# Kernel optimization log

Hardware: AMD Instinct MI355X
Metric: run time of the kernel (lower is better)

## Reference

```python
import jax, jax.numpy as jnp
import numpy as np

BOS = 1          # BOS_TOK_IDX
PAD = 0          # PAD_TOK_IDX (embedding padding row zeroed)
NL = 2           # n_layers (both decoder and encoder)
H_DEC = 1024     # decoder hidden = enc.emb_size
H_ENC = 512      # encoder hidden per direction (out_size = 1024)


def lstm_cell(x, h, c, Wih, Whh, bih, bhh):
    # PyTorch gate order: i, f, g, o
    gates = x @ Wih.T + h @ Whh.T + bih + bhh
    i, f, g, o = jnp.split(gates, 4, axis=-1)
    c = jax.nn.sigmoid(f) * c + jax.nn.sigmoid(i) * jnp.tanh(g)
    h = jax.nn.sigmoid(o) * jnp.tanh(c)
    return h, c


def setup_inputs() -> dict:
    key = jax.random.key(0)
    ks = jax.random.split(key, 20)
    B, T_ENC, V, E = 32, 128, 32000, 512
    sd = 1.0 / np.sqrt(H_DEC)
    se = 1.0 / np.sqrt(H_ENC)
    u = lambda k, shape, s: jax.random.uniform(k, shape, jnp.float32, -s, s)
    emb_W = jax.random.normal(ks[0], (V, E), jnp.float32)
    emb_W = emb_W.at[PAD].set(0.0)  # padding_idx
    return {
        "enc_outs": jax.random.normal(ks[1], (B, T_ENC, 2 * H_ENC), jnp.float32),
        "enc_h": 0.1 * jax.random.normal(ks[2], (NL, B, H_DEC), jnp.float32),
        "enc_c": 0.1 * jax.random.normal(ks[3], (NL, B, H_DEC), jnp.float32),
        "max_len": 256,
        "emb_W": emb_W,
        # decoder LSTM (unidirectional, 2 layers; layer0 in=E, layer1 in=H_DEC)
        "dec_Wih0": u(ks[4], (4 * H_DEC, E), sd),
        "dec_Whh0": u(ks[5], (4 * H_DEC, H_DEC), sd),
        "dec_bih0": u(ks[6], (4 * H_DEC,), sd),
        "dec_bhh0": u(ks[7], (4 * H_DEC,), sd),
        "dec_Wih1": u(ks[8], (4 * H_DEC, H_DEC), sd),
        "dec_Whh1": u(ks[9], (4 * H_DEC, H_DEC), sd),
        "dec_bih1": u(ks[10], (4 * H_DEC,), sd),
        "dec_bhh1": u(ks[11], (4 * H_DEC,), sd),
        # encoder biLSTM, stacked [layer, dir]; input dim 1024 for both layers
        "enc_Wih": u(ks[12], (NL, 2, 4 * H_ENC, 2 * H_ENC), se),
        "enc_Whh": u(ks[13], (NL, 2, 4 * H_ENC, H_ENC), se),
        "enc_bih": u(ks[14], (NL, 2, 4 * H_ENC), se),
        "enc_bhh": u(ks[15], (NL, 2, 4 * H_ENC), se),
    }


def _run_dir(x, Wih, Whh, bih, bhh, reverse):
    # x: [B, T, D] -> ys: [B, T, H], final (h, c)
    B = x.shape[0]
    H = Whh.shape[-1]
    z = jnp.zeros((B, H), dtype=x.dtype)

    def step(carry, xt):
        h, c = lstm_cell(xt, carry[0], carry[1], Wih, Whh, bih, bhh)
        return (h, c), h

    (hT, cT), ys = jax.lax.scan(step, (z, z), jnp.swapaxes(x, 0, 1), reverse=reverse)
    return jnp.swapaxes(ys, 0, 1), hT, cT


def reference(enc_outs, enc_h, enc_c, max_len, emb_W,
              dec_Wih0, dec_Whh0, dec_bih0, dec_bhh0,
              dec_Wih1, dec_Whh1, dec_bih1, dec_bhh1,
              enc_Wih, enc_Whh, enc_bih, enc_bhh):
    B = enc_outs.shape[0]
    # dec_inps is never updated in the loop: always the BOS embedding (eval dropout = id)
    x0 = jnp.broadcast_to(emb_W[BOS], (B, emb_W.shape[1]))

    def dec_step(carry, _):
        h0, c0, h1, c1 = carry
        h0, c0 = lstm_cell(x0, h0, c0, dec_Wih0, dec_Whh0, dec_bih0, dec_bhh0)
        h1, c1 = lstm_cell(h0, h1, c1, dec_Wih1, dec_Whh1, dec_bih1, dec_bhh1)
        return (h0, c0, h1, c1), h1

    init = (enc_h[0], enc_c[0], enc_h[1], enc_c[1])
    _, result = jax.lax.scan(dec_step, init, None, length=max_len)  # [T, B, H_DEC]
    out = jnp.swapaxes(result, 0, 1)  # [B, T, H_DEC]

    # bidirectional encoder over the decoded sequence (pre_embedded, full lengths)
    for l in range(NL):
        yf, hf, cf = _run_dir(out, enc_Wih[l, 0], enc_Whh[l, 0], enc_bih[l, 0], enc_bhh[l, 0], False)
        yb, hb, cb = _run_dir(out, enc_Wih[l, 1], enc_Whh[l, 1], enc_bih[l, 1], enc_bhh[l, 1], True)
        out = jnp.concatenate([yf, yb], axis=-1)

    # to_dec_state: concat last-layer fwd/bwd states, expand over n_layers
    lnhn = jnp.concatenate([hf, hb], axis=1)  # [B, out_size]
    lncn = jnp.concatenate([cf, cb], axis=1)
    dec_h = jnp.broadcast_to(lnhn, (NL,) + lnhn.shape)
    dec_c = jnp.broadcast_to(lncn, (NL,) + lncn.shape)
    return out, dec_h, dec_c
```

## Files before the change

kernel.cpp:

```cpp
#include <hip/hip_runtime.h>


typedef _Float16 f16;
typedef _Float16 hvec8 __attribute__((ext_vector_type(8)));
typedef float fvec4 __attribute__((ext_vector_type(4)));

#define WS_H0   4096
#define WS_H1   135168
#define WS_HE   266240
#define WS_DEC  397312
#define WS_Y0   17174528

__device__ __forceinline__ fvec4 mf(hvec8 a, hvec8 b, fvec4 c) {
    return __builtin_amdgcn_mfma_f32_16x16x32_f16(a, b, c, 0, 0, 0);
}

__device__ __forceinline__ hvec8 ldb8(const float* p) {
    hvec8 h;
#pragma unroll
    for (int j = 0; j < 8; ++j) h[j] = (f16)p[j];
    return h;
}

__device__ __forceinline__ hvec8 lda8(const f16* p) {
    hvec8 v;
    asm volatile("global_load_dwordx4 %0, %1, off sc1" : "=v"(v) : "v"(p));
    return v;
}
__device__ __forceinline__ void vm_wait() {
    asm volatile("s_waitcnt vmcnt(0)" ::: "memory");
    __builtin_amdgcn_sched_barrier(0);
}

__device__ __forceinline__ void st2(f16* p, float a, float b) {
    union { f16 h[2]; unsigned u; } x;
    x.h[0] = (f16)a; x.h[1] = (f16)b;
    __hip_atomic_store((unsigned*)p, x.u, __ATOMIC_RELAXED, __HIP_MEMORY_SCOPE_AGENT);
}

__device__ __forceinline__ float sigf(float x) { return 1.f / (1.f + __expf(-x)); }
__device__ __forceinline__ float thf(float x) {
    x = fminf(15.f, fmaxf(-15.f, x));
    float e = __expf(2.f * x);
    return (e - 1.f) / (e + 1.f);
}

#define RED(t, m, w, n)  red[(((t)*16 + (m))*132) + ((w)*16) + (n)]

__device__ __forceinline__ float sum8(const float* p) {
    return ((p[0] + p[16]) + (p[32] + p[48])) + ((p[64] + p[80]) + (p[96] + p[112]));
}

__global__ void __launch_bounds__(512, 1)
seq2seq_kernel(const float* __restrict__ enc_h, const float* __restrict__ enc_c,
               const float* __restrict__ emb_W,
               const float* __restrict__ dWih0, const float* __restrict__ dWhh0,
               const float* __restrict__ dbih0, const float* __restrict__ dbhh0,
               const float* __restrict__ dWih1, const float* __restrict__ dWhh1,
               const float* __restrict__ dbih1, const float* __restrict__ dbhh1,
               const float* __restrict__ eWih, const float* __restrict__ eWhh,
               const float* __restrict__ ebih, const float* __restrict__ ebhh,
               float* __restrict__ out, char* __restrict__ ws)
{
    const int tid  = threadIdx.x;
    const int wave = tid >> 6, lane = tid & 63;
    const int wg   = blockIdx.x;
    const int bg   = wg >> 7;
    const int g    = wg & 127;
    const int n16  = lane & 15;
    const int kq   = (lane >> 4) * 8;

    unsigned* flags  = (unsigned*)(out + 8388608);
    unsigned* myflag = flags + (size_t)wg * 64;

    f16* H0  = (f16*)(ws + WS_H0);
    f16* H1  = (f16*)(ws + WS_H1);
    f16* HE  = (f16*)(ws + WS_HE);
    f16* DEC = (f16*)(ws + WS_DEC);
    f16* Y0  = (f16*)(ws + WS_Y0);

    __shared__ float red[64 * 132];
    __shared__ float cdec[2][8][16];
    __shared__ float cenc[16][16];
    __shared__ float pre0_l[32];
    __shared__ float bias1_l[32];
    __shared__ float biasE_l[64];

    unsigned cnt = 0;
    auto barpoll = [&](int base, int width, unsigned tgt) {
        if (lane == 0)
            __hip_atomic_store(myflag, tgt, __ATOMIC_RELAXED, __HIP_MEMORY_SCOPE_AGENT);
        const unsigned* p0 = flags + (size_t)(base + (lane & (width - 1))) * 64;
        for (;;) {
            unsigned a = __hip_atomic_load(p0, __ATOMIC_RELAXED, __HIP_MEMORY_SCOPE_AGENT);
            if (width > 64) {
                unsigned b = __hip_atomic_load(p0 + 64 * 64, __ATOMIC_RELAXED, __HIP_MEMORY_SCOPE_AGENT);
                a = a < b ? a : b;
                if (width > 128) {
                    unsigned c2 = __hip_atomic_load(p0 + 128 * 64, __ATOMIC_RELAXED, __HIP_MEMORY_SCOPE_AGENT);
                    unsigned d2 = __hip_atomic_load(p0 + 192 * 64, __ATOMIC_RELAXED, __HIP_MEMORY_SCOPE_AGENT);
                    a = a < c2 ? a : c2;
                    a = a < d2 ? a : d2;
                }
            }
            if (__all((int)(a >= tgt))) break;
            __builtin_amdgcn_s_sleep(1);
        }
    };

    const int u0 = g * 8;
    hvec8 bL0[2][4], bL1[2][8];
    {
        const int gate = n16 >> 2, uu = n16 & 3;
#pragma unroll
        for (int t = 0; t < 2; ++t) {
            const int r = gate * 1024 + u0 + t * 4 + uu;
#pragma unroll
            for (int s = 0; s < 4; ++s)
                bL0[t][s] = ldb8(dWhh0 + (size_t)r * 1024 + wave * 128 + s * 32 + kq);
#pragma unroll
            for (int s = 0; s < 8; ++s) {
                const int k1 = wave * 256 + s * 32;
                bL1[t][s] = (k1 < 1024)
                    ? ldb8(dWih1 + (size_t)r * 1024 + k1 + kq)
                    : ldb8(dWhh1 + (size_t)r * 1024 + (k1 - 1024) + kq);
            }
        }
    }
    if (tid < 128) {
        const int which = tid >> 6, q = tid & 63, j = q >> 4, m = q & 15;
        const int b = bg * 16 + m, u = u0 + 2 * j;
        const float* src_c = enc_c + (size_t)(which * 32 + b) * 1024 + u;
        const float* src_h = enc_h + (size_t)(which * 32 + b) * 1024 + u;
        cdec[which][2 * j][m]     = src_c[0];
        cdec[which][2 * j + 1][m] = src_c[1];
        f16* dst = which ? H1 : H0;
        st2(dst + (size_t)(32 + b) * 1024 + u, src_h[0], src_h[1]);
    }
    if (tid < 32) {
        const int t = tid >> 4, nn = tid & 15;
        const int r = (nn >> 2) * 1024 + u0 + t * 4 + (nn & 3);
        const float* x0 = emb_W + 512;
        float s = dbih0[r] + dbhh0[r];
        const float* wr = dWih0 + (size_t)r * 512;
        for (int k = 0; k < 512; ++k) s += wr[k] * x0[k];
        pre0_l[tid]  = s;
        bias1_l[tid] = dbih1[r] + dbhh1[r];
    }
    __syncthreads();
    if (wave == 0) barpoll(bg * 128, 128, ++cnt);
    __syncthreads();

    for (int tau = 0; tau <= 256; ++tau) {
        const int prd = (tau + 1) & 1;
        const int pwr = tau & 1;
        fvec4 acc[4];
#pragma unroll
        for (int i = 0; i < 4; ++i) acc[i] = 0;
        const int m = n16;
        hvec8 a0f[4], a1f[8];
        if (tau < 256) {
            const f16* a0 = H0 + (size_t)(prd * 32 + bg * 16 + m) * 1024 + wave * 128 + kq;
#pragma unroll
            for (int s = 0; s < 4; ++s) a0f[s] = lda8(a0 + s * 32);
        }
        if (tau >= 1) {
            const f16* a1 = (wave < 4)
                ? H0 + (size_t)(prd * 32 + bg * 16 + m) * 1024 + wave * 256 + kq
                : H1 + (size_t)(pwr * 32 + bg * 16 + m) * 1024 + (wave - 4) * 256 + kq;
#pragma unroll
            for (int s = 0; s < 8; ++s) a1f[s] = lda8(a1 + s * 32);
        }
        vm_wait();
        if (tau < 256) {
#pragma unroll
            for (int s = 0; s < 4; ++s) {
                acc[0] = mf(a0f[s], bL0[0][s], acc[0]);
                acc[1] = mf(a0f[s], bL0[1][s], acc[1]);
            }
        }
        if (tau >= 1) {
#pragma unroll
            for (int s = 0; s < 8; ++s) {
                acc[2] = mf(a1f[s], bL1[0][s], acc[2]);
                acc[3] = mf(a1f[s], bL1[1][s], acc[3]);
            }
        }
        {
            const int mg = lane >> 4;
#pragma unroll
            for (int t = 0; t < 4; ++t)
#pragma unroll
                for (int r = 0; r < 4; ++r)
                    RED(t, mg * 4 + r, wave, n16) = acc[t][r];
        }
        __syncthreads();
        float s0 = 0.f, s1 = 0.f;
        int   sm2 = 0, sj = 0;
        if (wave == 1 && tau < 256) {
            const int q = tid - 64;
            const int j = q >> 4, m2 = q & 15, t = j >> 1;
            float hh[2];
#pragma unroll
            for (int e = 0; e < 2; ++e) {
                const int uu = 2 * j + e, ul = uu & 3;
                const float* p = &RED(t, m2, 0, ul);
                const float gi = sum8(p)      + pre0_l[t * 16 + ul];
                const float gf = sum8(p + 4)  + pre0_l[t * 16 + 4 + ul];
                const float gg = sum8(p + 8)  + pre0_l[t * 16 + 8 + ul];
                const float go = sum8(p + 12) + pre0_l[t * 16 + 12 + ul];
                float c = cdec[0][uu][m2];
                c = sigf(gf) * c + sigf(gi) * thf(gg);
                hh[e] = sigf(go) * thf(c);
                cdec[0][uu][m2] = c;
            }
            st2(H0 + (size_t)(pwr * 32 + bg * 16 + m2) * 1024 + u0 + 2 * j, hh[0], hh[1]);
        }
        if (wave == 2 && tau >= 1) {
            const int q = tid - 128;
            const int j = q >> 4, m2 = q & 15, t = j >> 1;
            float hh[2];
#pragma unroll
            for (int e = 0; e < 2; ++e) {
                const int uu = 2 * j + e, ul = uu & 3;
                const float* p = &RED(2 + t, m2, 0, ul);
                const float gi = sum8(p)      + bias1_l[t * 16 + ul];
                const float gf = sum8(p + 4)  + bias1_l[t * 16 + 4 + ul];
                const float gg = sum8(p + 8)  + bias1_l[t * 16 + 8 + ul];
                const float go = sum8(p + 12) + bias1_l[t * 16 + 12 + ul];
                float c = cdec[1][uu][m2];
                c = sigf(gf) * c + sigf(gi) * thf(gg);
                hh[e] = sigf(go) * thf(c);
                cdec[1][uu][m2] = c;
            }
            const int b = bg * 16 + m2, u = u0 + 2 * j;
            st2(H1 + (size_t)(prd * 32 + b) * 1024 + u, hh[0], hh[1]);
            s0 = hh[0]; s1 = hh[1]; sm2 = m2; sj = j;
        }
        __syncthreads();
        if (wave == 0) {
            barpoll(bg * 128, 128, ++cnt);
        } else if (wave == 2 && tau >= 1) {
            st2(DEC + ((size_t)(tau - 1) * 32 + bg * 16 + sm2) * 1024 + u0 + 2 * sj, s0, s1);
        }
        __syncthreads();
    }

    __syncthreads();
    if (wave == 0) barpoll(0, 256, ++cnt);
    __syncthreads();
    if (wg >= 128) return;

    const int bg2 = wg >> 6;
    const int dir = (wg >> 5) & 1;
    const int ge  = wg & 31;
    const int ue0 = ge * 16;
    const int dbase = bg2 * 64 + dir * 32;
    float fdh0 = 0.f, fdh1 = 0.f, fdc0 = 0.f, fdc1 = 0.f;
    int   fdm2 = 0, fdj = 0;
    for (int l = 0; l < 2; ++l) {
        hvec8 bE[4][6];
        {
            const int gate = n16 >> 2, uu = n16 & 3;
            const float* Wih = eWih + (size_t)(l * 2 + dir) * 2048 * 1024;
            const float* Whh = eWhh + (size_t)(l * 2 + dir) * 2048 * 512;
#pragma unroll
            for (int t = 0; t < 4; ++t) {
                const int r = gate * 512 + ue0 + t * 4 + uu;
#pragma unroll
                for (int s = 0; s < 6; ++s) {
                    const int kb = wave * 192 + s * 32;
                    bE[t][s] = (kb < 1024)
                        ? ldb8(Wih + (size_t)r * 1024 + kb + kq)
                        : ldb8(Whh + (size_t)r * 512 + (kb - 1024) + kq);
                }
            }
        }
        if (tid < 64) {
            const int t = tid >> 4, nn = tid & 15;
            const int r = (nn >> 2) * 512 + ue0 + t * 4 + (nn & 3);
            biasE_l[tid] = ebih[(size_t)(l * 2 + dir) * 2048 + r]
                         + ebhh[(size_t)(l * 2 + dir) * 2048 + r];
        }
        if (tid < 128) {
            const int j = tid >> 4, m = tid & 15;
            cenc[2 * j][m] = 0.f;
            cenc[2 * j + 1][m] = 0.f;
            st2(HE + (size_t)((dir * 2 + 1) * 32 + bg2 * 16 + m) * 512 + ue0 + 2 * j, 0.f, 0.f);
        }
        __syncthreads();
        if (wave == 0) barpoll(dbase, 32, ++cnt);
        __syncthreads();
        const f16* yprev = (l == 0) ? DEC : Y0;
        hvec8 ypf[6];
        {
            const int t0 = dir ? 255 : 0;
            const int b = bg2 * 16 + n16;
#pragma unroll
            for (int s = 0; s < 6; ++s) {
                const int kb = wave * 192 + s * 32;
                if (kb < 1024)
                    ypf[s] = lda8(yprev + ((size_t)t0 * 32 + b) * 1024 + kb + kq);
            }
        }
        for (int tau = 0; tau < 256; ++tau) {
            const int t = dir ? (255 - tau) : tau;
            const int prd = (tau + 1) & 1, pwr = tau & 1;
            const int b = bg2 * 16 + n16;
            hvec8 hef[6];
#pragma unroll
            for (int s = 0; s < 6; ++s) {
                const int kb = wave * 192 + s * 32;
                if (kb >= 1024)
                    hef[s] = lda8(HE + (size_t)((dir * 2 + prd) * 32 + b) * 512 + (kb - 1024) + kq);
            }
            vm_wait();
            fvec4 acc2[4];
#pragma unroll
            for (int i = 0; i < 4; ++i) acc2[i] = 0;
#pragma unroll
            for (int s = 0; s < 6; ++s) {
                const int kb = wave * 192 + s * 32;
                const hvec8 a = (kb < 1024) ? ypf[s] : hef[s];
                acc2[0] = mf(a, bE[0][s], acc2[0]);
                acc2[1] = mf(a, bE[1][s], acc2[1]);
                acc2[2] = mf(a, bE[2][s], acc2[2]);
                acc2[3] = mf(a, bE[3][s], acc2[3]);
            }
            if (tau < 255) {
                const int tn = dir ? (t - 1) : (t + 1);
#pragma unroll
                for (int s = 0; s < 6; ++s) {
                    const int kb = wave * 192 + s * 32;
                    if (kb < 1024)
                        ypf[s] = lda8(yprev + ((size_t)tn * 32 + b) * 1024 + kb + kq);
                }
            }
            const int mg = lane >> 4;
#pragma unroll
            for (int tt = 0; tt < 4; ++tt)
#pragma unroll
                for (int r = 0; r < 4; ++r)
                    RED(tt, mg * 4 + r, wave, n16) = acc2[tt][r];
            __syncthreads();
            float dh0 = 0.f, dh1 = 0.f, dc0 = 0.f, dc1 = 0.f;
            int   dm2 = 0, dj = 0;
            if (tid >= 64 && tid < 192) {
                const int q = tid - 64;
                const int j = q >> 4, m2 = q & 15;
                float hh[2], cc[2];
#pragma unroll
                for (int e = 0; e < 2; ++e) {
                    const int uu = 2 * j + e, tt = uu >> 2, ul = uu & 3;
                    const float* p = &RED(tt, m2, 0, ul);
                    const float gi = sum8(p)      + biasE_l[tt * 16 + ul];
                    const float gf = sum8(p + 4)  + biasE_l[tt * 16 + 4 + ul];
                    const float gg = sum8(p + 8)  + biasE_l[tt * 16 + 8 + ul];
                    const float go = sum8(p + 12) + biasE_l[tt * 16 + 12 + ul];
                    float c = cenc[uu][m2];
                    c = sigf(gf) * c + sigf(gi) * thf(gg);
                    hh[e] = sigf(go) * thf(c);
                    cc[e] = c;
                    cenc[uu][m2] = c;
                }
                st2(HE + (size_t)((dir * 2 + pwr) * 32 + bg2 * 16 + m2) * 512 + ue0 + 2 * j,
                    hh[0], hh[1]);
                dh0 = hh[0]; dh1 = hh[1]; dc0 = cc[0]; dc1 = cc[1];
                dm2 = m2; dj = j;
            }
            __syncthreads();
            if (wave == 0) {
                if (!(l == 1 && tau == 255)) barpoll(dbase, 32, ++cnt);
            } else if (tid >= 64 && tid < 192) {
                const int b2 = bg2 * 16 + dm2, u = ue0 + 2 * dj;
                if (l == 0) {
                    st2(Y0 + ((size_t)t * 32 + b2) * 1024 + dir * 512 + u, dh0, dh1);
                } else {
                    float* o = out + ((size_t)b2 * 256 + t) * 1024 + dir * 512 + u;
                    o[0] = dh0; o[1] = dh1;
                    if (tau == 255) {
                        fdh0 = dh0; fdh1 = dh1;
                        fdc0 = dc0; fdc1 = dc1;
                        fdm2 = dm2; fdj = dj;
                    }
                }
            }
            __syncthreads();
        }
        if (l == 0) {
            __syncthreads();
            if (wave == 0) barpoll(bg2 * 64, 64, ++cnt);
            __syncthreads();
        }
    }
    __syncthreads();
    if (wave == 0) barpoll(0, 128, ++cnt);
    __syncthreads();
    if (tid >= 64 && tid < 192) {
        const int b2 = bg2 * 16 + fdm2;
        const int col = dir * 512 + ue0 + 2 * fdj;
        float* oh = out + 8388608 + (size_t)b2 * 1024 + col;
        float* oc = out + 8454144 + (size_t)b2 * 1024 + col;
        oh[0] = fdh0; oh[1] = fdh1;
        oh[32768] = fdh0; oh[32769] = fdh1;
        oc[0] = fdc0; oc[1] = fdc1;
        oc[32768] = fdc0; oc[32769] = fdc1;
    }
}

extern "C" void kernel_launch(void* const* d_in, const int* in_sizes, int n_in,
                              void* d_out, int out_size, void* d_ws, size_t ws_size,
                              hipStream_t stream) {
    (void)in_sizes; (void)n_in; (void)out_size; (void)ws_size;
    const float* enc_h = (const float*)d_in[1];
    const float* enc_c = (const float*)d_in[2];
    const float* emb_W = (const float*)d_in[4];
    const float* dWih0 = (const float*)d_in[5];
    const float* dWhh0 = (const float*)d_in[6];
    const float* dbih0 = (const float*)d_in[7];
    const float* dbhh0 = (const float*)d_in[8];
    const float* dWih1 = (const float*)d_in[9];
    const float* dWhh1 = (const float*)d_in[10];
    const float* dbih1 = (const float*)d_in[11];
    const float* dbhh1 = (const float*)d_in[12];
    const float* eWih  = (const float*)d_in[13];
    const float* eWhh  = (const float*)d_in[14];
    const float* ebih  = (const float*)d_in[15];
    const float* ebhh  = (const float*)d_in[16];
    float* outp = (float*)d_out;
    char* ws = (char*)d_ws;

    hipMemsetAsync((char*)d_out + 33554432, 0, 65536, stream);

    void* args[] = {&enc_h, &enc_c, &emb_W, &dWih0, &dWhh0, &dbih0, &dbhh0,
                    &dWih1, &dWhh1, &dbih1, &dbhh1, &eWih, &eWhh, &ebih, &ebhh,
                    &outp, &ws};
    hipLaunchCooperativeKernel((const void*)seq2seq_kernel, dim3(256), dim3(512),
                               args, 0, stream);
}
```

Baseline: 3.552 ms.

## Split decoder layers across separate workgroups with decoupled layer barriers

Workgroups in the decoder phase are now dedicated to a single LSTM layer, each covering 16 hidden units instead of both layers for 8 units. Layer-0 state is kept in a 4-deep ring buffer, so layer 0 can run up to two steps ahead of layer 1. Each step waits on its own layer's flags plus a lagged target on the other layer, rather than one barrier over all 128 workgroups. The aim is to shorten the critical path per timestep and balance per-workgroup work, at the cost of more flag polling and pipelined cross-layer dependencies.

```diff
diff --git a/kernel.cpp b/kernel.cpp
--- a/kernel.cpp
+++ b/kernel.cpp
@@ -5,7 +5,6 @@
 typedef _Float16 hvec8 __attribute__((ext_vector_type(8)));
 typedef float fvec4 __attribute__((ext_vector_type(4)));
 
-#define WS_H0   4096
 #define WS_H1   135168
 #define WS_HE   266240
 #define WS_DEC  397312
@@ -66,28 +65,27 @@
     const int wave = tid >> 6, lane = tid & 63;
     const int wg   = blockIdx.x;
     const int bg   = wg >> 7;
-    const int g    = wg & 127;
+    const int layer= (wg >> 6) & 1;
+    const int g2   = wg & 63;
     const int n16  = lane & 15;
     const int kq   = (lane >> 4) * 8;
+    const int m    = n16;
 
     unsigned* flags  = (unsigned*)(out + 8388608);
     unsigned* myflag = flags + (size_t)wg * 64;
 
-    f16* H0  = (f16*)(ws + WS_H0);
     f16* H1  = (f16*)(ws + WS_H1);
     f16* HE  = (f16*)(ws + WS_HE);
     f16* DEC = (f16*)(ws + WS_DEC);
     f16* Y0  = (f16*)(ws + WS_Y0);
+    f16* H0R = Y0;
 
     __shared__ float red[64 * 132];
-    __shared__ float cdec[2][8][16];
-    __shared__ float cenc[16][16];
-    __shared__ float pre0_l[32];
-    __shared__ float bias1_l[32];
-    __shared__ float biasE_l[64];
+    __shared__ float cst[16][16];
+    __shared__ float bias_l[64];
 
     unsigned cnt = 0;
-    auto barpoll = [&](int base, int width, unsigned tgt) {
+    auto barpollW = [&](int base, int width, unsigned tgt) {
         if (lane == 0)
             __hip_atomic_store(myflag, tgt, __ATOMIC_RELAXED, __HIP_MEMORY_SCOPE_AGENT);
         const unsigned* p0 = flags + (size_t)(base + (lane & (width - 1))) * 64;
@@ -107,83 +105,108 @@
             __builtin_amdgcn_s_sleep(1);
         }
     };
-
-    const int u0 = g * 8;
-    hvec8 bL0[2][4], bL1[2][8];
+    auto barpoll2 = [&](int ownbase, int othbase, unsigned tgt, unsigned otgt) {
+        if (lane == 0)
+            __hip_atomic_store(myflag, tgt, __ATOMIC_RELAXED, __HIP_MEMORY_SCOPE_AGENT);
+        const unsigned* p0 = flags + (size_t)(ownbase + lane) * 64;
+        const unsigned* q0 = flags + (size_t)(othbase + lane) * 64;
+        for (;;) {
+            unsigned a = __hip_atomic_load(p0, __ATOMIC_RELAXED, __HIP_MEMORY_SCOPE_AGENT);
+            unsigned b = __hip_atomic_load(q0, __ATOMIC_RELAXED, __HIP_MEMORY_SCOPE_AGENT);
+            if (__all((int)((a >= tgt) && (b >= otgt)))) break;
+            __builtin_amdgcn_s_sleep(1);
+        }
+    };
+
+    const int u0 = g2 * 16;
+    hvec8 bW[4][8];
     {
         const int gate = n16 >> 2, uu = n16 & 3;
-#pragma unroll
-        for (int t = 0; t < 2; ++t) {
-            const int r = gate * 1024 + u0 + t * 4 + uu;
-#pragma unroll
-            for (int s = 0; s < 4; ++s)
-                bL0[t][s] = ldb8(dWhh0 + (size_t)r * 1024 + wave * 128 + s * 32 + kq);
-#pragma unroll
-            for (int s = 0; s < 8; ++s) {
-                const int k1 = wave * 256 + s * 32;
-                bL1[t][s] = (k1 < 1024)
-                    ? ldb8(dWih1 + (size_t)r * 1024 + k1 + kq)
-                    : ldb8(dWhh1 + (size_t)r * 1024 + (k1 - 1024) + kq);
+        if (layer == 0) {
+#pragma unroll
+            for (int t = 0; t < 4; ++t) {
+                const int r = gate * 1024 + u0 + t * 4 + uu;
+#pragma unroll
+                for (int s = 0; s < 4; ++s)
+                    bW[t][s] = ldb8(dWhh0 + (size_t)r * 1024 + wave * 128 + s * 32 + kq);
+            }
+        } else {
+#pragma unroll
+            for (int t = 0; t < 4; ++t) {
+                const int r = gate * 1024 + u0 + t * 4 + uu;
+#pragma unroll
+                for (int s = 0; s < 8; ++s) {
+                    const int k1 = wave * 256 + s * 32;
+                    bW[t][s] = (k1 < 1024)
+                        ? ldb8(dWih1 + (size_t)r * 1024 + k1 + kq)
+                        : ldb8(dWhh1 + (size_t)r * 1024 + (k1 - 1024) + kq);
+                }
             }
         }
     }
     if (tid < 128) {
-        const int which = tid >> 6, q = tid & 63, j = q >> 4, m = q & 15;
-        const int b = bg * 16 + m, u = u0 + 2 * j;
-        const float* src_c = enc_c + (size_t)(which * 32 + b) * 1024 + u;
-        const float* src_h = enc_h + (size_t)(which * 32 + b) * 1024 + u;
-        cdec[which][2 * j][m]     = src_c[0];
-        cdec[which][2 * j + 1][m] = src_c[1];
-        f16* dst = which ? H1 : H0;
-        st2(dst + (size_t)(32 + b) * 1024 + u, src_h[0], src_h[1]);
-    }
-    if (tid < 32) {
+        const int j = tid >> 4, mm = tid & 15;
+        const int b = bg * 16 + mm, u = u0 + 2 * j;
+        const float* sc = enc_c + (size_t)(layer * 32 + b) * 1024 + u;
+        const float* sh = enc_h + (size_t)(layer * 32 + b) * 1024 + u;
+        cst[2 * j][mm]     = sc[0];
+        cst[2 * j + 1][mm] = sc[1];
+        if (layer == 0) st2(H0R + (size_t)(3 * 32 + b) * 1024 + u, sh[0], sh[1]);
+        else            st2(H1  + (size_t)(32 + b) * 1024 + u, sh[0], sh[1]);
+    }
+    if (tid < 64) {
         const int t = tid >> 4, nn = tid & 15;
         const int r = (nn >> 2) * 1024 + u0 + t * 4 + (nn & 3);
-        const float* x0 = emb_W + 512;
-        float s = dbih0[r] + dbhh0[r];
-        const float* wr = dWih0 + (size_t)r * 512;
-        for (int k = 0; k < 512; ++k) s += wr[k] * x0[k];
-        pre0_l[tid]  = s;
-        bias1_l[tid] = dbih1[r] + dbhh1[r];
-    }
+        if (layer == 0) {
+            const float* x0 = emb_W + 512;
+            float s = dbih0[r] + dbhh0[r];
+            const float* wr = dWih0 + (size_t)r * 512;
+            for (int k = 0; k < 512; ++k) s += wr[k] * x0[k];
+            bias_l[tid] = s;
+        } else {
+            bias_l[tid] = dbih1[r] + dbhh1[r];
+        }
+    }
+    const int L0base = bg * 128, L1base = bg * 128 + 64;
+    const int ownbase = layer ? L1base : L0base;
+    const int othbase = layer ? L0base : L1base;
     __syncthreads();
-    if (wave == 0) barpoll(bg * 128, 128, ++cnt);
+    ++cnt;
+    if (wave == 0) barpoll2(ownbase, othbase, cnt, cnt);
     __syncthreads();
 
-    for (int tau = 0; tau <= 256; ++tau) {
-        const int prd = (tau + 1) & 1;
-        const int pwr = tau & 1;
+    for (int n = 0; n <= 256; ++n) {
+        const int prd = (n + 1) & 1;
+        const int pwr = n & 1;
+        const bool act = layer ? (n >= 1) : (n < 256);
         fvec4 acc[4];
 #pragma unroll
         for (int i = 0; i < 4; ++i) acc[i] = 0;
-        const int m = n16;
-        hvec8 a0f[4], a1f[8];
-        if (tau < 256) {
-            const f16* a0 = H0 + (size_t)(prd * 32 + bg * 16 + m) * 1024 + wave * 128 + kq;
-#pragma unroll
-            for (int s = 0; s < 4; ++s) a0f[s] = lda8(a0 + s * 32);
-        }
-        if (tau >= 1) {
-            const f16* a1 = (wave < 4)
-                ? H0 + (size_t)(prd * 32 + bg * 16 + m) * 1024 + wave * 256 + kq
-                : H1 + (size_t)(pwr * 32 + bg * 16 + m) * 1024 + (wave - 4) * 256 + kq;
-#pragma unroll
-            for (int s = 0; s < 8; ++s) a1f[s] = lda8(a1 + s * 32);
-        }
-        vm_wait();
-        if (tau < 256) {
-#pragma unroll
-            for (int s = 0; s < 4; ++s) {
-                acc[0] = mf(a0f[s], bL0[0][s], acc[0]);
-                acc[1] = mf(a0f[s], bL0[1][s], acc[1]);
-            }
-        }
-        if (tau >= 1) {
-#pragma unroll
-            for (int s = 0; s < 8; ++s) {
-                acc[2] = mf(a1f[s], bL1[0][s], acc[2]);
-                acc[3] = mf(a1f[s], bL1[1][s], acc[3]);
+        if (act) {
+            hvec8 af[8];
+            if (layer == 0) {
+                const f16* a0 = H0R + (size_t)((((n - 1) & 3)) * 32 + bg * 16 + m) * 1024
+                              + wave * 128 + kq;
+#pragma unroll
+                for (int s = 0; s < 4; ++s) af[s] = lda8(a0 + s * 32);
+                vm_wait();
+#pragma unroll
+                for (int s = 0; s < 4; ++s)
+#pragma unroll
+                    for (int t = 0; t < 4; ++t) acc[t] = mf(af[s], bW[t][s], acc[t]);
+            } else {
+                const f16* b0 = H0R + (size_t)((((n - 1) & 3)) * 32 + bg * 16 + m) * 1024;
+                const f16* b1 = H1 + (size_t)(pwr * 32 + bg * 16 + m) * 1024;
+#pragma unroll
+                for (int s = 0; s < 8; ++s) {
+                    const int k1 = wave * 256 + s * 32;
+                    af[s] = lda8(k1 < 1024 ? b0 + k1 + kq : b1 + (k1 - 1024) + kq);
+                }
+                vm_wait();
+#pragma unroll
+                for (int s = 0; s < 8; ++s)
+#pragma unroll
+                    for (int t = 0; t < 4; ++t) acc[t] = mf(af[s], bW[t][s], acc[t]);
             }
         }
         {
@@ -191,63 +214,50 @@
 #pragma unroll
             for (int t = 0; t < 4; ++t)
 #pragma unroll
-                for (int r = 0; r < 4; ++r)
-                    RED(t, mg * 4 + r, wave, n16) = acc[t][r];
+                for (int r2 = 0; r2 < 4; ++r2)
+                    RED(t, mg * 4 + r2, wave, n16) = acc[t][r2];
         }
         __syncthreads();
         float s0 = 0.f, s1 = 0.f;
         int   sm2 = 0, sj = 0;
-        if (wave == 1 && tau < 256) {
+        if (tid >= 64 && tid < 192 && act) {
             const int q = tid - 64;
-            const int j = q >> 4, m2 = q & 15, t = j >> 1;
+            const int j = q >> 4, m2 = q & 15;
             float hh[2];
 #pragma unroll
             for (int e = 0; e < 2; ++e) {
-                const int uu = 2 * j + e, ul = uu & 3;
-                const float* p = &RED(t, m2, 0, ul);
-                const float gi = sum8(p)      + pre0_l[t * 16 + ul];
-                const float gf = sum8(p + 4)  + pre0_l[t * 16 + 4 + ul];
-                const float gg = sum8(p + 8)  + pre0_l[t * 16 + 8 + ul];
-                const float go = sum8(p + 12) + pre0_l[t * 16 + 12 + ul];
-                float c = cdec[0][uu][m2];
+                const int uu = 2 * j + e, tt = uu >> 2, ul = uu & 3;
+                const float* p = &RED(tt, m2, 0, ul);
+                const float gi = sum8(p)      + bias_l[tt * 16 + ul];
+                const float gf = sum8(p + 4)  + bias_l[tt * 16 + 4 + ul];
+                const float gg = sum8(p + 8)  + bias_l[tt * 16 + 8 + ul];
+                const float go = sum8(p + 12) + bias_l[tt * 16 + 12 + ul];
+                float c = cst[uu][m2];
                 c = sigf(gf) * c + sigf(gi) * thf(gg);
                 hh[e] = sigf(go) * thf(c);
-                cdec[0][uu][m2] = c;
-            }
-            st2(H0 + (size_t)(pwr * 32 + bg * 16 + m2) * 1024 + u0 + 2 * j, hh[0], hh[1]);
-        }
-        if (wave == 2 && tau >= 1) {
-            const int q = tid - 128;
-            const int j = q >> 4, m2 = q & 15, t = j >> 1;
-            float hh[2];
-#pragma unroll
-            for (int e = 0; e < 2; ++e) {
-                const int uu = 2 * j + e, ul = uu & 3;
-                const float* p = &RED(2 + t, m2, 0, ul);
-                const float gi = sum8(p)      + bias1_l[t * 16 + ul];
-                const float gf = sum8(p + 4)  + bias1_l[t * 16 + 4 + ul];
-                const float gg = sum8(p + 8)  + bias1_l[t * 16 + 8 + ul];
-                const float go = sum8(p + 12) + bias1_l[t * 16 + 12 + ul];
-                float c = cdec[1][uu][m2];
-                c = sigf(gf) * c + sigf(gi) * thf(gg);
-                hh[e] = sigf(go) * thf(c);
-                cdec[1][uu][m2] = c;
+                cst[uu][m2] = c;
             }
             const int b = bg * 16 + m2, u = u0 + 2 * j;
-            st2(H1 + (size_t)(prd * 32 + b) * 1024 + u, hh[0], hh[1]);
-            s0 = hh[0]; s1 = hh[1]; sm2 = m2; sj = j;
+            if (layer == 0) {
+                st2(H0R + (size_t)((n & 3) * 32 + b) * 1024 + u, hh[0], hh[1]);
+            } else {
+                st2(H1 + (size_t)(prd * 32 + b) * 1024 + u, hh[0], hh[1]);
+                s0 = hh[0]; s1 = hh[1]; sm2 = m2; sj = j;
+            }
         }
         __syncthreads();
+        ++cnt;
         if (wave == 0) {
-            barpoll(bg * 128, 128, ++cnt);
-        } else if (wave == 2 && tau >= 1) {
-            st2(DEC + ((size_t)(tau - 1) * 32 + bg * 16 + sm2) * 1024 + u0 + 2 * sj, s0, s1);
+            if (layer == 0) barpoll2(L0base, L1base, cnt, cnt < 2 ? 0u : cnt - 2);
+            else            barpoll2(L1base, L0base, cnt, cnt);
+        } else if (layer == 1 && tid >= 64 && tid < 192 && n >= 1) {
+            st2(DEC + ((size_t)(n - 1) * 32 + bg * 16 + sm2) * 1024 + u0 + 2 * sj, s0, s1);
         }
         __syncthreads();
     }
 
-    __syncthreads();
-    if (wave == 0) barpoll(0, 256, ++cnt);
+    ++cnt;
+    if (wave == 0) barpollW(0, 256, cnt);
     __syncthreads();
     if (wg >= 128) return;
 
@@ -279,17 +289,18 @@
         if (tid < 64) {
             const int t = tid >> 4, nn = tid & 15;
             const int r = (nn >> 2) * 512 + ue0 + t * 4 + (nn & 3);
-            biasE_l[tid] = ebih[(size_t)(l * 2 + dir) * 2048 + r]
-                         + ebhh[(size_t)(l * 2 + dir) * 2048 + r];
+            bias_l[tid] = ebih[(size_t)(l * 2 + dir) * 2048 + r]
+                        + ebhh[(size_t)(l * 2 + dir) * 2048 + r];
         }
         if (tid < 128) {
-            const int j = tid >> 4, m = tid & 15;
-            cenc[2 * j][m] = 0.f;
-            cenc[2 * j + 1][m] = 0.f;
-            st2(HE + (size_t)((dir * 2 + 1) * 32 + bg2 * 16 + m) * 512 + ue0 + 2 * j, 0.f, 0.f);
+            const int j = tid >> 4, mm = tid & 15;
+            cst[2 * j][mm] = 0.f;
+            cst[2 * j + 1][mm] = 0.f;
+            st2(HE + (size_t)((dir * 2 + 1) * 32 + bg2 * 16 + mm) * 512 + ue0 + 2 * j, 0.f, 0.f);
         }
         __syncthreads();
-        if (wave == 0) barpoll(dbase, 32, ++cnt);
+        ++cnt;
+        if (wave == 0) barpollW(dbase, 32, cnt);
         __syncthreads();
         const f16* yprev = (l == 0) ? DEC : Y0;
         hvec8 ypf[6];
@@ -340,8 +351,8 @@
 #pragma unroll
             for (int tt = 0; tt < 4; ++tt)
 #pragma unroll
-                for (int r = 0; r < 4; ++r)
-                    RED(tt, mg * 4 + r, wave, n16) = acc2[tt][r];
+                for (int r2 = 0; r2 < 4; ++r2)
+                    RED(tt, mg * 4 + r2, wave, n16) = acc2[tt][r2];
             __syncthreads();
             float dh0 = 0.f, dh1 = 0.f, dc0 = 0.f, dc1 = 0.f;
             int   dm2 = 0, dj = 0;
@@ -353,15 +364,15 @@
                 for (int e = 0; e < 2; ++e) {
                     const int uu = 2 * j + e, tt = uu >> 2, ul = uu & 3;
                     const float* p = &RED(tt, m2, 0, ul);
-                    const float gi = sum8(p)      + biasE_l[tt * 16 + ul];
-                    const float gf = sum8(p + 4)  + biasE_l[tt * 16 + 4 + ul];
-                    const float gg = sum8(p + 8)  + biasE_l[tt * 16 + 8 + ul];
-                    const float go = sum8(p + 12) + biasE_l[tt * 16 + 12 + ul];
-                    float c = cenc[uu][m2];
+                    const float gi = sum8(p)      + bias_l[tt * 16 + ul];
+                    const float gf = sum8(p + 4)  + bias_l[tt * 16 + 4 + ul];
+                    const float gg = sum8(p + 8)  + bias_l[tt * 16 + 8 + ul];
+                    const float go = sum8(p + 12) + bias_l[tt * 16 + 12 + ul];
+                    float c = cst[uu][m2];
                     c = sigf(gf) * c + sigf(gi) * thf(gg);
                     hh[e] = sigf(go) * thf(c);
                     cc[e] = c;
-                    cenc[uu][m2] = c;
+                    cst[uu][m2] = c;
                 }
                 st2(HE + (size_t)((dir * 2 + pwr) * 32 + bg2 * 16 + m2) * 512 + ue0 + 2 * j,
                     hh[0], hh[1]);
@@ -369,8 +380,9 @@
                 dm2 = m2; dj = j;
             }
             __syncthreads();
+            ++cnt;
             if (wave == 0) {
-                if (!(l == 1 && tau == 255)) barpoll(dbase, 32, ++cnt);
+                if (!(l == 1 && tau == 255)) barpollW(dbase, 32, cnt);
             } else if (tid >= 64 && tid < 192) {
                 const int b2 = bg2 * 16 + dm2, u = ue0 + 2 * dj;
                 if (l == 0) {
@@ -389,12 +401,14 @@
         }
         if (l == 0) {
             __syncthreads();
-            if (wave == 0) barpoll(bg2 * 64, 64, ++cnt);
+            ++cnt;
+            if (wave == 0) barpollW(bg2 * 64, 64, cnt);
             __syncthreads();
         }
     }
     __syncthreads();
-    if (wave == 0) barpoll(0, 128, ++cnt);
+    ++cnt;
+    if (wave == 0) barpollW(0, 128, cnt);
     __syncthreads();
     if (tid >= 64 && tid < 192) {
         const int b2 = bg2 * 16 + fdm2;
```

Result: faster. 3.146 ms (-11.4%).
